# Optimization experiments

Hardware: AMD Instinct MI355X
Metric: run time of the kernel (lower is better)

## Reference

```python
import jax, jax.numpy as jnp
import numpy as np

V, E, H, C = 50257, 256, 512, 16  # vocab, embed_dim, hidden_size, n_cells
B, T = 256, 128
LN_EPS = 1e-5


def setup_inputs() -> dict:
    key = jax.random.key(0)
    ks = jax.random.split(key, 16)
    s_h = 1.0 / np.sqrt(H)
    s_e = 1.0 / np.sqrt(E)
    return {
        "tokens": jax.random.randint(ks[0], (B, T), 0, V),
        "emb": jax.random.normal(ks[1], (V, E), jnp.float32) * 0.02,
        "Wproj": jax.random.normal(ks[2], (E, H), jnp.float32) * s_e,
        "bproj": jnp.zeros((H,), jnp.float32),
        "Wp": jax.random.normal(ks[3], (C, H, H), jnp.float32) * s_h,
        "bp": jnp.zeros((C, H), jnp.float32),
        "ln_g": jnp.ones((C, H), jnp.float32),
        "ln_b": jnp.zeros((C, H), jnp.float32),
        "Wih": jax.random.normal(ks[4], (C, 4 * H, H), jnp.float32) * s_h,
        "bih": jnp.zeros((C, 4 * H), jnp.float32),
        "Whh": jax.random.normal(ks[5], (C, 4 * H, H), jnp.float32) * s_h,
        "bhh": jnp.zeros((C, 4 * H), jnp.float32),
        "Wa": jax.random.normal(ks[6], (C, H, H), jnp.float32) * s_h,
        "ba": jnp.zeros((C, H), jnp.float32),
        "gate_logit": jnp.zeros((C,), jnp.float32),  # torch.tensor(0.0) per cell
    }


def _layernorm(x, g, b):
    mu = jnp.mean(x, axis=-1, keepdims=True)
    var = jnp.var(x, axis=-1, keepdims=True)
    return (x - mu) * jax.lax.rsqrt(var + LN_EPS) * g + b


def reference(tokens, emb, Wproj, bproj, Wp, bp, ln_g, ln_b,
              Wih, bih, Whh, bhh, Wa, ba, gate_logit):
    # embedding (padding_idx=0 zeroed) + projection to hidden size
    emb = emb.at[0].set(0.0)
    xs = emb[tokens] @ Wproj + bproj              # [B,T,H]
    xs = jnp.transpose(xs, (1, 0, 2))             # [T,B,H] for scan

    gate = jax.nn.sigmoid(gate_logit)[:, None, None]  # [C,1,1]

    def step(carry, x_t):
        h, c, ext = carry                          # h,c: [C,B,H], ext: [B,H]
        # input_adapter == Identity (input_size == hidden_size); external injection
        x = x_t[None] + 0.3 * ext[None]            # [C,B,H]
        # perception: Linear + ReLU + LayerNorm
        p = jax.nn.relu(jnp.einsum('cbh,chk->cbk', x, Wp) + bp[:, None, :])
        p = _layernorm(p, ln_g[:, None, :], ln_b[:, None, :])
        # LSTMCell (torch gate order i, f, g, o)
        gates = (jnp.einsum('cbh,cgh->cbg', p, Wih) + bih[:, None, :]
                 + jnp.einsum('cbh,cgh->cbg', h, Whh) + bhh[:, None, :])
        i_g, f_g, g_g, o_g = jnp.split(gates, 4, axis=-1)
        c_new = jax.nn.sigmoid(f_g) * c + jax.nn.sigmoid(i_g) * jnp.tanh(g_g)
        h_new = jax.nn.sigmoid(o_g) * jnp.tanh(c_new)
        # association + sigmoid gate
        a = jnp.tanh(jnp.einsum('cbh,chk->cbk', h_new, Wa) + ba[:, None, :])
        out = a * gate                             # [C,B,H]
        y = jnp.mean(out, axis=0)                  # aggregate cells -> [B,H]
        return (h_new, c_new, y), y

    h0 = jnp.zeros((C, B, H), xs.dtype)
    c0 = jnp.zeros((C, B, H), xs.dtype)
    ext0 = jnp.zeros((B, H), xs.dtype)
    _, ys = jax.lax.scan(step, (h0, c0, ext0), xs)  # ys: [T,B,H]
    return jnp.transpose(ys, (1, 0, 2))             # [B,T,H]
```

## Files before the change

kernel.cpp:

```cpp
#include <hip/hip_runtime.h>
#include <hip/hip_bf16.h>

#define V 50257
#define E 256
#define H 512
#define C 16
#define B 256
#define T 128

typedef _Float16 f16x8 __attribute__((ext_vector_type(8)));
typedef _Float16 f16x4 __attribute__((ext_vector_type(4)));
typedef float f32x4 __attribute__((ext_vector_type(4)));

__device__ __forceinline__ float sigm(float x) { return 1.0f / (1.0f + __expf(-x)); }

__device__ __forceinline__ void gload16(const _Float16* g, _Float16* l) {
  __builtin_amdgcn_global_load_lds((const __attribute__((address_space(1))) unsigned*)g,
                                   (__attribute__((address_space(3))) unsigned*)l, 16, 0, 0);
}

__global__ __launch_bounds__(256) void k_emb(const int* __restrict__ tokens,
                                             const float* __restrict__ emb,
                                             const float* __restrict__ Wproj,
                                             const float* __restrict__ bproj,
                                             _Float16* __restrict__ xs_h) {
  __shared__ float elds[16][256];
  const int tid = threadIdx.x;
  const int r0 = blockIdx.x * 16;
#pragma unroll
  for (int i = 0; i < 16; ++i) {
    int r = r0 + i;
    int t = r >> 8, b = r & 255;
    int tok = tokens[b * T + t];
    elds[i][tid] = (tok == 0) ? 0.0f : emb[(size_t)tok * E + tid];
  }
  __syncthreads();
  float acc0[16], acc1[16];
#pragma unroll
  for (int i = 0; i < 16; ++i) { acc0[i] = 0.0f; acc1[i] = 0.0f; }
  for (int k = 0; k < E; k += 4) {
    float w0[4], w1[4];
#pragma unroll
    for (int kk = 0; kk < 4; ++kk) {
      w0[kk] = Wproj[(k + kk) * H + tid];
      w1[kk] = Wproj[(k + kk) * H + tid + 256];
    }
#pragma unroll
    for (int i = 0; i < 16; ++i) {
      float4 e4 = *(const float4*)&elds[i][k];
      acc0[i] = fmaf(e4.x, w0[0], acc0[i]);
      acc0[i] = fmaf(e4.y, w0[1], acc0[i]);
      acc0[i] = fmaf(e4.z, w0[2], acc0[i]);
      acc0[i] = fmaf(e4.w, w0[3], acc0[i]);
      acc1[i] = fmaf(e4.x, w1[0], acc1[i]);
      acc1[i] = fmaf(e4.y, w1[1], acc1[i]);
      acc1[i] = fmaf(e4.z, w1[2], acc1[i]);
      acc1[i] = fmaf(e4.w, w1[3], acc1[i]);
    }
  }
  float bp0 = bproj[tid], bp1 = bproj[tid + 256];
#pragma unroll
  for (int i = 0; i < 16; ++i) {
    size_t r = (size_t)(r0 + i);
    xs_h[r * H + tid] = (_Float16)(acc0[i] + bp0);
    xs_h[r * H + tid + 256] = (_Float16)(acc1[i] + bp1);
  }
}

__global__ __launch_bounds__(256) void k_cvt_wg(const float* __restrict__ Wih,
                                                const float* __restrict__ Whh,
                                                _Float16* __restrict__ WgT) {
  for (size_t i4 = ((size_t)blockIdx.x * 256 + threadIdx.x) * 4; i4 < (size_t)33554432;
       i4 += (size_t)gridDim.x * 1024) {
    size_t c = i4 >> 21;
    size_t rem = i4 & 2097151;
    size_t np = rem >> 10;
    size_t k2 = rem & 1023;
    int gate = (int)((np >> 4) & 3);
    int hh = (int)(((np >> 6) << 4) | (np & 15));
    size_t n = (size_t)gate * 512 + hh;
    const float* src = (k2 < 512) ? (Wih + (c * 2048 + n) * 512 + k2)
                                  : (Whh + (c * 2048 + n) * 512 + (k2 - 512));
    float4 v = *(const float4*)src;
    f16x4 o;
    o[0] = (_Float16)v.x; o[1] = (_Float16)v.y; o[2] = (_Float16)v.z; o[3] = (_Float16)v.w;
    *(f16x4*)&WgT[i4] = o;
  }
}

__global__ __launch_bounds__(256) void k_cvt_tr(const float* __restrict__ W,
                                                _Float16* __restrict__ WT) {
  __shared__ float tl[64][65];
  const int tid = threadIdx.x;
  const int c = blockIdx.z;
  const int k0 = blockIdx.y * 64, n0 = blockIdx.x * 64;
  const float* Wc = W + (size_t)c * 262144;
#pragma unroll
  for (int q = 0; q < 16; ++q) {
    int idx = q * 256 + tid;
    int r = idx >> 6, cc = idx & 63;
    tl[r][cc] = Wc[(size_t)(k0 + r) * 512 + n0 + cc];
  }
  __syncthreads();
  _Float16* WTc = WT + (size_t)c * 262144;
#pragma unroll
  for (int q = 0; q < 16; ++q) {
    int idx = q * 256 + tid;
    int rr = idx >> 6, cc = idx & 63;
    WTc[(size_t)(n0 + rr) * 512 + k0 + cc] = (_Float16)tl[cc][rr];
  }
}

__global__ __launch_bounds__(256) void k_bias(const float* __restrict__ bih,
                                              const float* __restrict__ bhh,
                                              float* __restrict__ bsum) {
  int i = blockIdx.x * 256 + threadIdx.x;
  if (i < C * 4 * H) {
    int c = i >> 11, np = i & 2047;
    int gate = (np >> 4) & 3;
    int hh = ((np >> 6) << 4) | (np & 15);
    int n = gate * 512 + hh;
    bsum[i] = bih[c * 2048 + n] + bhh[c * 2048 + n];
  }
}

__global__ __launch_bounds__(256, 2) void k_pln(const _Float16* __restrict__ xq,
                                                const _Float16* __restrict__ WpT,
                                                const float* __restrict__ bp,
                                                const float* __restrict__ ln_g,
                                                const float* __restrict__ ln_b,
                                                _Float16* __restrict__ Pdst) {
  __shared__ _Float16 Bsl[512 * 64];
  const int tid = threadIdx.x;
  const int w = tid >> 6, l = tid & 63;
  const int blk = blockIdx.x;
  const int c = blk & 15;
  const int mt = blk >> 4;
  const int m0 = mt * 32;
  const _Float16* Bb = WpT + (size_t)c * 262144;
  const int srow = l >> 3, sj = l & 7;
  const int lm = l & 15, lk = l >> 4;
  f32x4 acc[2][8];
#pragma unroll
  for (int i = 0; i < 2; ++i)
#pragma unroll
    for (int j = 0; j < 8; ++j) acc[i][j] = (f32x4)0.0f;
  const _Float16* pA0 = xq + (size_t)(m0 + lm) * 512 + lk * 8;
  const _Float16* pA1 = pA0 + 16 * 512;
  f16x8 a0s0 = *(const f16x8*)pA0;
  f16x8 a0s1 = *(const f16x8*)(pA0 + 32);
  f16x8 a1s0 = *(const f16x8*)pA1;
  f16x8 a1s1 = *(const f16x8*)(pA1 + 32);
#pragma unroll 1
  for (int kb = 0; kb < 8; ++kb) {
#pragma unroll
    for (int q = 0; q < 16; ++q) {
      int r = q * 32 + w * 8 + srow;
      int gj = sj ^ (r & 7);
      gload16(Bb + (size_t)r * 512 + kb * 64 + gj * 8, &Bsl[(q * 32 + w * 8) * 64]);
    }
    f16x8 u00 = a0s0, u01 = a0s1, u10 = a1s0, u11 = a1s1;
    if (kb < 7) {
      a0s0 = *(const f16x8*)(pA0 + (kb + 1) * 64);
      a0s1 = *(const f16x8*)(pA0 + (kb + 1) * 64 + 32);
      a1s0 = *(const f16x8*)(pA1 + (kb + 1) * 64);
      a1s1 = *(const f16x8*)(pA1 + (kb + 1) * 64 + 32);
    }
    __syncthreads();
#pragma unroll
    for (int s2 = 0; s2 < 2; ++s2) {
      f16x8 bf[8];
#pragma unroll
      for (int j = 0; j < 8; ++j) {
        int RN = w * 128 + j * 16 + lm;
        int pn = (s2 * 4 + lk) ^ (RN & 7);
        bf[j] = *(const f16x8*)&Bsl[RN * 64 + pn * 8];
      }
      f16x8 ua = s2 ? u01 : u00;
      f16x8 ub = s2 ? u11 : u10;
#pragma unroll
      for (int j = 0; j < 8; ++j) {
        acc[0][j] = __builtin_amdgcn_mfma_f32_16x16x32_f16(ua, bf[j], acc[0][j], 0, 0, 0);
        acc[1][j] = __builtin_amdgcn_mfma_f32_16x16x32_f16(ub, bf[j], acc[1][j], 0, 0, 0);
      }
    }
    __syncthreads();
  }
  float bv[8], gcol[8], bcol[8];
#pragma unroll
  for (int j = 0; j < 8; ++j) {
    int col = w * 128 + j * 16 + lm;
    bv[j] = bp[c * 512 + col];
    gcol[j] = ln_g[c * 512 + col];
    bcol[j] = ln_b[c * 512 + col];
  }
  float vals[2][8][4];
  float s1l[2][4], s2l[2][4];
#pragma unroll
  for (int i = 0; i < 2; ++i)
#pragma unroll
    for (int rg = 0; rg < 4; ++rg) { s1l[i][rg] = 0.0f; s2l[i][rg] = 0.0f; }
#pragma unroll
  for (int i = 0; i < 2; ++i)
#pragma unroll
    for (int j = 0; j < 8; ++j)
#pragma unroll
      for (int rg = 0; rg < 4; ++rg) {
        float v = fmaxf(acc[i][j][rg] + bv[j], 0.0f);
        vals[i][j][rg] = v;
        s1l[i][rg] += v;
        s2l[i][rg] += v * v;
      }
#pragma unroll
  for (int m = 1; m < 16; m <<= 1) {
#pragma unroll
    for (int i = 0; i < 2; ++i)
#pragma unroll
      for (int rg = 0; rg < 4; ++rg) {
        s1l[i][rg] += __shfl_xor(s1l[i][rg], m, 64);
        s2l[i][rg] += __shfl_xor(s2l[i][rg], m, 64);
      }
  }
  float* st = (float*)Bsl;
  if (lm == 0) {
#pragma unroll
    for (int i = 0; i < 2; ++i)
#pragma unroll
      for (int rg = 0; rg < 4; ++rg) {
        int row = i * 16 + lk * 4 + rg;
        st[(w * 32 + row) * 2] = s1l[i][rg];
        st[(w * 32 + row) * 2 + 1] = s2l[i][rg];
      }
  }
  __syncthreads();
  float mu_[2][4], rs_[2][4];
#pragma unroll
  for (int i = 0; i < 2; ++i)
#pragma unroll
    for (int rg = 0; rg < 4; ++rg) {
      int row = i * 16 + lk * 4 + rg;
      float t1 = 0.0f, t2 = 0.0f;
#pragma unroll
      for (int ww = 0; ww < 4; ++ww) {
        t1 += st[(ww * 32 + row) * 2];
        t2 += st[(ww * 32 + row) * 2 + 1];
      }
      float mu = t1 * (1.0f / 512.0f);
      float var = t2 * (1.0f / 512.0f) - mu * mu;
      mu_[i][rg] = mu;
      rs_[i][rg] = rsqrtf(var + 1e-5f);
    }
#pragma unroll
  for (int i = 0; i < 2; ++i)
#pragma unroll
    for (int j = 0; j < 8; ++j) {
      int col = w * 128 + j * 16 + lm;
#pragma unroll
      for (int rg = 0; rg < 4; ++rg) {
        int row = i * 16 + lk * 4 + rg;
        float o = (vals[i][j][rg] - mu_[i][rg]) * rs_[i][rg] * gcol[j] + bcol[j];
        Pdst[((size_t)c * 256 + m0 + row) * 1024 + col] = (_Float16)o;
      }
    }
}

__global__ __launch_bounds__(256, 2) void k_gates(const _Float16* __restrict__ A,
                                                  const _Float16* __restrict__ Bm,
                                                  const float* __restrict__ bias,
                                                  float* __restrict__ cstate,
                                                  _Float16* __restrict__ hdst) {
  __shared__ _Float16 Asl[256 * 64];
  __shared__ _Float16 Bsl[64 * 64];
  const int tid = threadIdx.x;
  const int w = tid >> 6, l = tid & 63;
  const int blk = blockIdx.x;
  const int c = blk & 15;
  const int n0 = (blk >> 4) * 64;
  const _Float16* Ab = A + (size_t)c * 262144;
  const _Float16* Bb = Bm + (size_t)c * 2097152 + (size_t)n0 * 1024;
  f32x4 acc[4][4];
#pragma unroll
  for (int i = 0; i < 4; ++i)
#pragma unroll
    for (int j = 0; j < 4; ++j) acc[i][j] = (f32x4)0.0f;
  const int wm = w * 64;
  const int srow = l >> 3, sj = l & 7;
  const int lm = l & 15, lk = l >> 4;
#pragma unroll 1
  for (int kb = 0; kb < 16; ++kb) {
#pragma unroll
    for (int q = 0; q < 8; ++q) {
      int r = w * 64 + q * 8 + srow;
      int gj = sj ^ (r & 7);
      gload16(Ab + (size_t)r * 1024 + kb * 64 + gj * 8, &Asl[(w * 64 + q * 8) * 64]);
    }
#pragma unroll
    for (int q = 0; q < 2; ++q) {
      int r = w * 16 + q * 8 + srow;
      int gj = sj ^ (r & 7);
      gload16(Bb + (size_t)r * 1024 + kb * 64 + gj * 8, &Bsl[(w * 16 + q * 8) * 64]);
    }
    __syncthreads();
#pragma unroll
    for (int s2 = 0; s2 < 2; ++s2) {
      f16x8 af[4], bf[4];
#pragma unroll
      for (int i = 0; i < 4; ++i) {
        int R = wm + i * 16 + lm;
        int p = (s2 * 4 + lk) ^ (R & 7);
        af[i] = *(const f16x8*)&Asl[R * 64 + p * 8];
      }
#pragma unroll
      for (int j = 0; j < 4; ++j) {
        int RN = j * 16 + lm;
        int pn = (s2 * 4 + lk) ^ (RN & 7);
        bf[j] = *(const f16x8*)&Bsl[RN * 64 + pn * 8];
      }
#pragma unroll
      for (int i = 0; i < 4; ++i)
#pragma unroll
        for (int j = 0; j < 4; ++j)
          acc[i][j] = __builtin_amdgcn_mfma_f32_16x16x32_f16(af[i], bf[j], acc[i][j], 0, 0, 0);
    }
    __syncthreads();
  }
  const int rl = lk * 4, cl = lm;
  const int hh = ((n0 >> 6) << 4) + cl;
  float bv[4];
#pragma unroll
  for (int j = 0; j < 4; ++j) bv[j] = bias[(size_t)c * 2048 + n0 + j * 16 + cl];
#pragma unroll
  for (int i = 0; i < 4; ++i) {
#pragma unroll
    for (int rg = 0; rg < 4; ++rg) {
      int row = wm + i * 16 + rl + rg;
      float ig = acc[i][0][rg] + bv[0];
      float fg = acc[i][1][rg] + bv[1];
      float gg = acc[i][2][rg] + bv[2];
      float og = acc[i][3][rg] + bv[3];
      size_t ci = ((size_t)c * 256 + row) * 512 + hh;
      float cn = sigm(fg) * cstate[ci] + sigm(ig) * tanhf(gg);
      cstate[ci] = cn;
      hdst[((size_t)c * 256 + row) * 1024 + 512 + hh] = (_Float16)(sigm(og) * tanhf(cn));
    }
  }
}

__global__ __launch_bounds__(256, 2) void k_assoc(const _Float16* __restrict__ An,
                                                  const _Float16* __restrict__ WaT,
                                                  const float* __restrict__ ba,
                                                  const float* __restrict__ gl,
                                                  _Float16* __restrict__ abuf) {
  __shared__ _Float16 Asl[64 * 64];
  __shared__ _Float16 Bsl[128 * 64];
  const int tid = threadIdx.x;
  const int w = tid >> 6, l = tid & 63;
  const int blk = blockIdx.x;
  const int c = blk & 15;
  const int r_ = blk >> 4;
  const int nt = r_ & 3, mt = r_ >> 2;
  const int n0 = nt * 128;
  const _Float16* Ab = An + 512 + ((size_t)c * 256 + mt * 64) * 1024;
  const _Float16* Bb = WaT + (size_t)c * 262144 + (size_t)n0 * 512;
  f32x4 acc[2][4];
#pragma unroll
  for (int i = 0; i < 2; ++i)
#pragma unroll
    for (int j = 0; j < 4; ++j) acc[i][j] = (f32x4)0.0f;
  const int wm = (w >> 1) * 32, wn = (w & 1) * 64;
  const int srow = l >> 3, sj = l & 7;
  const int lm = l & 15, lk = l >> 4;
#pragma unroll 1
  for (int kb = 0; kb < 8; ++kb) {
#pragma unroll
    for (int q = 0; q < 2; ++q) {
      int r = q * 32 + w * 8 + srow;
      int gj = sj ^ (r & 7);
      gload16(Ab + (size_t)r * 1024 + kb * 64 + gj * 8, &Asl[(q * 32 + w * 8) * 64]);
    }
#pragma unroll
    for (int q = 0; q < 4; ++q) {
      int r = q * 32 + w * 8 + srow;
      int gj = sj ^ (r & 7);
      gload16(Bb + (size_t)r * 512 + kb * 64 + gj * 8, &Bsl[(q * 32 + w * 8) * 64]);
    }
    __syncthreads();
#pragma unroll
    for (int s2 = 0; s2 < 2; ++s2) {
      f16x8 af[2], bf[4];
#pragma unroll
      for (int i = 0; i < 2; ++i) {
        int R = wm + i * 16 + lm;
        int p = (s2 * 4 + lk) ^ (R & 7);
        af[i] = *(const f16x8*)&Asl[R * 64 + p * 8];
      }
#pragma unroll
      for (int j = 0; j < 4; ++j) {
        int RN = wn + j * 16 + lm;
        int pn = (s2 * 4 + lk) ^ (RN & 7);
        bf[j] = *(const f16x8*)&Bsl[RN * 64 + pn * 8];
      }
#pragma unroll
      for (int i = 0; i < 2; ++i)
#pragma unroll
        for (int j = 0; j < 4; ++j)
          acc[i][j] = __builtin_amdgcn_mfma_f32_16x16x32_f16(af[i], bf[j], acc[i][j], 0, 0, 0);
    }
    __syncthreads();
  }
  float gv = sigm(gl[c]);
#pragma unroll
  for (int i = 0; i < 2; ++i)
#pragma unroll
    for (int j = 0; j < 4; ++j) {
      int gc = n0 + wn + j * 16 + lm;
      float bav = ba[c * 512 + gc];
#pragma unroll
      for (int rg = 0; rg < 4; ++rg) {
        int row = mt * 64 + wm + i * 16 + lk * 4 + rg;
        float v = tanhf(acc[i][j][rg] + bav) * gv;
        abuf[(size_t)c * 131072 + (size_t)row * 512 + gc] = (_Float16)v;
      }
    }
}

__global__ __launch_bounds__(256) void k_agg(const _Float16* __restrict__ abuf,
                                             const _Float16* __restrict__ xs_h,
                                             _Float16* __restrict__ xq,
                                             float* __restrict__ out, int t) {
  int idx = blockIdx.x * 256 + threadIdx.x;
  int i4 = idx * 4;
  float s[4] = {0.0f, 0.0f, 0.0f, 0.0f};
#pragma unroll
  for (int c = 0; c < 16; ++c) {
    f16x4 a = *(const f16x4*)&abuf[(size_t)c * 131072 + i4];
#pragma unroll
    for (int j = 0; j < 4; ++j) s[j] += (float)a[j];
  }
  int b = i4 >> 9, h = i4 & 511;
  float4 y4;
  float* yp = &y4.x;
#pragma unroll
  for (int j = 0; j < 4; ++j) yp[j] = s[j] * (1.0f / 16.0f);
  *(float4*)&out[((size_t)b * T + t) * 512 + h] = y4;
  if (t + 1 < T) {
    f16x4 xs4 = *(const f16x4*)&xs_h[(size_t)(t + 1) * 131072 + i4];
    f16x4 xn;
#pragma unroll
    for (int j = 0; j < 4; ++j) xn[j] = (_Float16)((float)xs4[j] + 0.3f * yp[j]);
    *(f16x4*)&xq[i4] = xn;
  }
}

extern "C" void kernel_launch(void* const* d_in, const int* in_sizes, int n_in,
                              void* d_out, int out_size, void* d_ws, size_t ws_size,
                              hipStream_t stream) {
  const int* tokens = (const int*)d_in[0];
  const float* emb = (const float*)d_in[1];
  const float* Wproj = (const float*)d_in[2];
  const float* bproj = (const float*)d_in[3];
  const float* Wp = (const float*)d_in[4];
  const float* bp = (const float*)d_in[5];
  const float* ln_g = (const float*)d_in[6];
  const float* ln_b = (const float*)d_in[7];
  const float* Wih = (const float*)d_in[8];
  const float* bih = (const float*)d_in[9];
  const float* Whh = (const float*)d_in[10];
  const float* bhh = (const float*)d_in[11];
  const float* Wa = (const float*)d_in[12];
  const float* ba = (const float*)d_in[13];
  const float* gl = (const float*)d_in[14];
  float* out = (float*)d_out;

  char* w8 = (char*)d_ws;
  _Float16* xs_h = (_Float16*)w8;
  _Float16* Aq0 = (_Float16*)(w8 + 33554432);
  _Float16* Aq1 = (_Float16*)(w8 + 50331648);
  float* cbuf = (float*)(w8 + 67108864);
  _Float16* abuf = (_Float16*)(w8 + 75497472);
  _Float16* xq = (_Float16*)(w8 + 79691776);
  _Float16* WpT = (_Float16*)(w8 + 79953920);
  _Float16* WaT = (_Float16*)(w8 + 88342528);
  _Float16* WgT = (_Float16*)(w8 + 96731136);
  float* bsum = (float*)(w8 + 163840000);

  hipMemsetAsync(Aq0, 0, 16777216, stream);
  hipMemsetAsync(cbuf, 0, 8388608, stream);

  k_cvt_wg<<<4096, 256, 0, stream>>>(Wih, Whh, WgT);
  k_cvt_tr<<<dim3(8, 8, 16), 256, 0, stream>>>(Wp, WpT);
  k_cvt_tr<<<dim3(8, 8, 16), 256, 0, stream>>>(Wa, WaT);
  k_bias<<<128, 256, 0, stream>>>(bih, bhh, bsum);
  k_emb<<<T * B / 16, 256, 0, stream>>>(tokens, emb, Wproj, bproj, xs_h);
  hipMemcpyAsync(xq, xs_h, 262144, hipMemcpyDeviceToDevice, stream);

  for (int t = 0; t < T; ++t) {
    _Float16* Ac = (t & 1) ? Aq1 : Aq0;
    _Float16* An = (t & 1) ? Aq0 : Aq1;
    k_pln<<<128, 256, 0, stream>>>(xq, WpT, bp, ln_g, ln_b, Ac);
    k_gates<<<512, 256, 0, stream>>>(Ac, WgT, bsum, cbuf, An);
    k_assoc<<<256, 256, 0, stream>>>(An, WaT, ba, gl, abuf);
    k_agg<<<128, 256, 0, stream>>>(abuf, xs_h, xq, out, t);
  }
}
```

Baseline: 7.816 ms.

## Triple-buffer k_gates LDS loads and widen the block tile to 256x128

k_gates now runs 512-thread blocks with 8 waves in a 4x2 arrangement, each block computing a 256x128 output tile, so the grid shrinks from 512 to 256 blocks. The inner K loop gains a three-stage LDS ring filled by asynchronous global_load_lds, with explicit vmcnt waits and raw s_barrier so loads for later stages overlap the MFMA work on the current one. The aim is to hide global memory latency and to halve how often the A operand is reloaded. In exchange it needs about 147KB of LDS per block, allowing only one block per CU, and correctness now depends on hand-counted vmcnt values.

```diff
diff --git a/kernel.cpp b/kernel.cpp
--- a/kernel.cpp
+++ b/kernel.cpp
@@ -264,18 +264,17 @@
     }
 }
 
-__global__ __launch_bounds__(256, 2) void k_gates(const _Float16* __restrict__ A,
+__global__ __launch_bounds__(512, 1) void k_gates(const _Float16* __restrict__ A,
                                                   const _Float16* __restrict__ Bm,
                                                   const float* __restrict__ bias,
                                                   float* __restrict__ cstate,
                                                   _Float16* __restrict__ hdst) {
-  __shared__ _Float16 Asl[256 * 64];
-  __shared__ _Float16 Bsl[64 * 64];
+  __shared__ _Float16 sm[3 * 24576];
   const int tid = threadIdx.x;
   const int w = tid >> 6, l = tid & 63;
   const int blk = blockIdx.x;
   const int c = blk & 15;
-  const int n0 = (blk >> 4) * 64;
+  const int n0 = (blk >> 4) * 128;
   const _Float16* Ab = A + (size_t)c * 262144;
   const _Float16* Bb = Bm + (size_t)c * 2097152 + (size_t)n0 * 1024;
   f32x4 acc[4][4];
@@ -283,24 +282,47 @@
   for (int i = 0; i < 4; ++i)
 #pragma unroll
     for (int j = 0; j < 4; ++j) acc[i][j] = (f32x4)0.0f;
-  const int wm = w * 64;
+  const int wm = (w >> 1) * 64;
+  const int wn = (w & 1) * 64;
   const int srow = l >> 3, sj = l & 7;
   const int lm = l & 15, lk = l >> 4;
+
+  auto STAGE = [&](int buf, int kb) {
+    _Float16* As = sm + buf * 24576;
+    _Float16* Bs = As + 16384;
+#pragma unroll
+    for (int q = 0; q < 4; ++q) {
+      int rb = q * 64 + w * 8;
+      int r = rb + srow;
+      int gj = sj ^ (r & 7);
+      gload16(Ab + (size_t)r * 1024 + kb * 64 + gj * 8, &As[rb * 64]);
+    }
+#pragma unroll
+    for (int q = 0; q < 2; ++q) {
+      int rb = q * 64 + w * 8;
+      int r = rb + srow;
+      int gj = sj ^ (r & 7);
+      gload16(Bb + (size_t)r * 1024 + kb * 64 + gj * 8, &Bs[rb * 64]);
+    }
+  };
+
+  STAGE(0, 0);
+  STAGE(1, 1);
 #pragma unroll 1
   for (int kb = 0; kb < 16; ++kb) {
-#pragma unroll
-    for (int q = 0; q < 8; ++q) {
-      int r = w * 64 + q * 8 + srow;
-      int gj = sj ^ (r & 7);
-      gload16(Ab + (size_t)r * 1024 + kb * 64 + gj * 8, &Asl[(w * 64 + q * 8) * 64]);
-    }
-#pragma unroll
-    for (int q = 0; q < 2; ++q) {
-      int r = w * 16 + q * 8 + srow;
-      int gj = sj ^ (r & 7);
-      gload16(Bb + (size_t)r * 1024 + kb * 64 + gj * 8, &Bsl[(w * 16 + q * 8) * 64]);
-    }
-    __syncthreads();
+    const int cur = kb % 3;
+    if (kb + 2 < 16) STAGE((kb + 2) % 3, kb + 2);
+    if (kb < 14) {
+      asm volatile("s_waitcnt vmcnt(12)" ::: "memory");
+    } else if (kb == 14) {
+      asm volatile("s_waitcnt vmcnt(6)" ::: "memory");
+    } else {
+      asm volatile("s_waitcnt vmcnt(0)" ::: "memory");
+    }
+    __builtin_amdgcn_s_barrier();
+    __builtin_amdgcn_sched_barrier(0);
+    const _Float16* As = sm + cur * 24576;
+    const _Float16* Bs = As + 16384;
 #pragma unroll
     for (int s2 = 0; s2 < 2; ++s2) {
       f16x8 af[4], bf[4];
@@ -308,13 +330,10 @@
       for (int i = 0; i < 4; ++i) {
         int R = wm + i * 16 + lm;
         int p = (s2 * 4 + lk) ^ (R & 7);
-        af[i] = *(const f16x8*)&Asl[R * 64 + p * 8];
-      }
-#pragma unroll
-      for (int j = 0; j < 4; ++j) {
-        int RN = j * 16 + lm;
+        af[i] = *(const f16x8*)&As[R * 64 + p * 8];
+        int RN = wn + i * 16 + lm;
         int pn = (s2 * 4 + lk) ^ (RN & 7);
-        bf[j] = *(const f16x8*)&Bsl[RN * 64 + pn * 8];
+        bf[i] = *(const f16x8*)&Bs[RN * 64 + pn * 8];
       }
 #pragma unroll
       for (int i = 0; i < 4; ++i)
@@ -322,13 +341,14 @@
         for (int j = 0; j < 4; ++j)
           acc[i][j] = __builtin_amdgcn_mfma_f32_16x16x32_f16(af[i], bf[j], acc[i][j], 0, 0, 0);
     }
-    __syncthreads();
+    asm volatile("s_waitcnt lgkmcnt(0)" ::: "memory");
+    __builtin_amdgcn_s_barrier();
   }
   const int rl = lk * 4, cl = lm;
-  const int hh = ((n0 >> 6) << 4) + cl;
+  const int hh = (((n0 + wn) >> 6) << 4) + cl;
   float bv[4];
 #pragma unroll
-  for (int j = 0; j < 4; ++j) bv[j] = bias[(size_t)c * 2048 + n0 + j * 16 + cl];
+  for (int j = 0; j < 4; ++j) bv[j] = bias[(size_t)c * 2048 + (n0 + wn) + j * 16 + cl];
 #pragma unroll
   for (int i = 0; i < 4; ++i) {
 #pragma unroll
@@ -498,7 +518,7 @@
     _Float16* Ac = (t & 1) ? Aq1 : Aq0;
     _Float16* An = (t & 1) ? Aq0 : Aq1;
     k_pln<<<128, 256, 0, stream>>>(xq, WpT, bp, ln_g, ln_b, Ac);
-    k_gates<<<512, 256, 0, stream>>>(Ac, WgT, bsum, cbuf, An);
+    k_gates<<<256, 512, 0, stream>>>(Ac, WgT, bsum, cbuf, An);
     k_assoc<<<256, 256, 0, stream>>>(An, WaT, ba, gl, abuf);
     k_agg<<<128, 256, 0, stream>>>(abuf, xs_h, xq, out, t);
   }
```

Measured after the change: 7.611 ms. -2.6%, faster.
